# Performance work log

Measured on AMD Instinct MI355X. Metric: run time of the kernel, lower is better.

The kernel has to match this reference:

```python
import jax, jax.numpy as jnp
import numpy as np
import math

NUM_LEVEL = 16
LEVEL_DIM = 2
BASE_RES = 16
LOG2_T = 19
LEVEL_SCALE = 1.38191288
N_POINTS = 262144

_PRIMES = np.array([1, 2654435761, 805459861], dtype=np.uint32)  # tiny-cuda-nn hash primes
_CORNERS = np.array([[(c >> d) & 1 for d in range(3)] for c in range(8)], dtype=np.uint32)  # [8,3]


def _grid_meta():
    # mirrors GridEncoder.get_grid_info: per-level table offsets (aligned to 8)
    max_len = 2 ** LOG2_T
    offs = []
    off = 0
    for i in range(NUM_LEVEL):
        res = int(np.ceil(BASE_RES * LEVEL_SCALE ** i))
        p = min(max_len, res ** 3)
        p = int(np.ceil(p / 8) * 8)
        offs.append(off)
        off += p
    offs.append(off)
    return offs


def setup_inputs() -> dict:
    key = jax.random.key(0)
    k1, k2 = jax.random.split(key)
    offs = _grid_meta()
    # raw coords in [-1, 1); forward maps (x+1)/2 -> [0, 1)
    input_means = jax.random.uniform(k1, (N_POINTS, 3), dtype=jnp.float32) * 2.0 - 1.0
    # embeddings.data.uniform_(-0.01, 0.01)
    embeddings = jax.random.uniform(k2, (offs[-1], LEVEL_DIM), dtype=jnp.float32) * 0.02 - 0.01
    return {"input_means": input_means, "embeddings": embeddings}


def _encode(input_means, embeddings):
    x = (input_means + 1.0) / 2.0  # [N,3] in [0,1]
    offs = _grid_meta()
    lg_scale = math.log2(LEVEL_SCALE)
    corners = jnp.asarray(_CORNERS)  # [8,3]
    primes = jnp.asarray(_PRIMES)    # [3]
    outs = []
    for l in range(NUM_LEVEL):
        hsize = offs[l + 1] - offs[l]                    # table rows this level
        scale = 2.0 ** (l * lg_scale) * BASE_RES - 1.0   # align_corners=True
        res = int(math.ceil(scale)) + 1                  # grid resolution
        table = embeddings[offs[l]:offs[l + 1]]          # [hsize, C]
        pos = x * scale                                  # align_corners -> no +0.5
        pg = jnp.floor(pos)
        frac = pos - pg                                  # [N,3]
        pgu = pg.astype(jnp.uint32)
        cpos = pgu[:, None, :] + corners[None]           # [N,8,3] corner coords
        if res ** 3 > hsize:
            # hashed level: xor of coord*prime (uint32 wraparound)
            h = cpos * primes
            idx = h[..., 0] ^ h[..., 1] ^ h[..., 2]
        else:
            # dense (tiled) level
            r = jnp.uint32(res)
            idx = cpos[..., 0] + cpos[..., 1] * r + cpos[..., 2] * r * r
        idx = (idx % jnp.uint32(hsize)).astype(jnp.int32)
        feats = table[idx]                               # [N,8,C] gather
        w = jnp.where(corners[None] == 1, frac[:, None, :], 1.0 - frac[:, None, :]).prod(-1)  # [N,8]
        outs.append(jnp.einsum('nk,nkc->nc', w, feats))  # trilinear interp
    # matches ot_encod.permute(1,0,2).reshape(N, L*C): level-major feature concat
    return jnp.concatenate(outs, axis=-1)                # [N, L*C]


def reference(input_means, embeddings):
    return _encode(input_means, embeddings)
```

## Files before the change

kernel.cpp:

```cpp
#include <hip/hip_runtime.h>
#include <cmath>

#define NPTS 262144
#define NLVL 16
#define NDENSE 5
#define NHASH 11
#define HASH_MASK 0x7FFFFu
#define P2 2654435761u
#define P3 805459861u

typedef float v2f __attribute__((ext_vector_type(2)));
typedef float v3f __attribute__((ext_vector_type(3)));
typedef float v4f __attribute__((ext_vector_type(4)));
typedef float v4f8 __attribute__((ext_vector_type(4), aligned(8)));

struct MetaD { float scale[NDENSE]; unsigned off[NDENSE]; unsigned res[NDENSE]; };
struct MetaH { float scale[NHASH]; unsigned off[NHASH]; };

struct Pt { float x, y, z; };
struct Prep { unsigned idx[8]; float fx, fy, fz; };

__device__ __forceinline__ Pt load_pt_nt(const float* __restrict__ means, int p) {
    const v3f m = __builtin_nontemporal_load((const v3f*)(means + 3 * p));
    Pt q;
    q.x = (m.x + 1.0f) * 0.5f;
    q.y = (m.y + 1.0f) * 0.5f;
    q.z = (m.z + 1.0f) * 0.5f;
    return q;
}

__device__ __forceinline__ Prep hprep(Pt q, float s, unsigned off) {
    const float px = q.x * s, py = q.y * s, pz = q.z * s;
    const float gx = floorf(px), gy = floorf(py), gz = floorf(pz);
    Prep d;
    d.fx = px - gx; d.fy = py - gy; d.fz = pz - gz;
    const unsigned ix = (unsigned)gx, iy = (unsigned)gy, iz = (unsigned)gz;
    const unsigned hy0 = iy * P2, hy1 = hy0 + P2;
    const unsigned hz0 = iz * P3, hz1 = hz0 + P3;
    const unsigned h0 = hy0 ^ hz0, h1 = hy1 ^ hz0, h2 = hy0 ^ hz1, h3 = hy1 ^ hz1;
    d.idx[0] = ((ix ^ h0) & HASH_MASK) + off; d.idx[1] = (((ix + 1u) ^ h0) & HASH_MASK) + off;
    d.idx[2] = ((ix ^ h1) & HASH_MASK) + off; d.idx[3] = (((ix + 1u) ^ h1) & HASH_MASK) + off;
    d.idx[4] = ((ix ^ h2) & HASH_MASK) + off; d.idx[5] = (((ix + 1u) ^ h2) & HASH_MASK) + off;
    d.idx[6] = ((ix ^ h3) & HASH_MASK) + off; d.idx[7] = (((ix + 1u) ^ h3) & HASH_MASK) + off;
    return d;
}

__device__ __forceinline__ v2f trilerp(const v2f* f, float fx, float fy, float fz) {
    const float wx0 = 1.0f - fx, wy0 = 1.0f - fy, wz0 = 1.0f - fz;
    const float w00 = wz0 * wy0, w01 = wz0 * fy, w10 = fz * wy0, w11 = fz * fy;
    return w00 * (wx0 * f[0] + fx * f[1]) + w01 * (wx0 * f[2] + fx * f[3])
         + w10 * (wx0 * f[4] + fx * f[5]) + w11 * (wx0 * f[6] + fx * f[7]);
}

__global__ __launch_bounds__(256) void enc_hash(
    const float* __restrict__ means, const float* __restrict__ emb,
    v2f* __restrict__ dst, int lvl_major, MetaH meta)
{
    const unsigned b = blockIdx.x;
    const unsigned xcd = b & 7u, slot = b >> 3;
    unsigned il, chunk;
    if (slot < 512u) { il = xcd; chunk = slot; }
    else {
        const unsigned g = xcd * 192u + (slot - 512u);
        il = 8u + (g >> 9);
        chunk = g & 511u;
    }
    const float s = meta.scale[il];
    const unsigned off = meta.off[il];
    const unsigned lvl = il + NDENSE;
    const int p0 = (int)(chunk * 512u + threadIdx.x);
    const v2f* __restrict__ emb2 = (const v2f*)emb;

    const Prep A = hprep(load_pt_nt(means, p0), s, off);
    v2f fa[8];
#pragma unroll
    for (int k = 0; k < 8; ++k) fa[k] = emb2[A.idx[k]];
    const Prep B = hprep(load_pt_nt(means, p0 + 256), s, off);
    v2f fb[8];
#pragma unroll
    for (int k = 0; k < 8; ++k) fb[k] = emb2[B.idx[k]];

    const v2f ra = trilerp(fa, A.fx, A.fy, A.fz);
    const size_t diA = lvl_major ? ((size_t)lvl * NPTS + p0) : ((size_t)p0 * NLVL + lvl);
    dst[diA] = ra;
    const v2f rb = trilerp(fb, B.fx, B.fy, B.fz);
    const size_t diB = lvl_major ? ((size_t)lvl * NPTS + (p0 + 256)) : ((size_t)(p0 + 256) * NLVL + lvl);
    dst[diB] = rb;
}

__global__ __launch_bounds__(256) void finalize(
    const float* __restrict__ means, const float* __restrict__ emb,
    const v2f* __restrict__ ws, float* __restrict__ out, MetaD meta)
{
    const int p = blockIdx.x * 256 + threadIdx.x;

    v2f h[NHASH];
#pragma unroll
    for (int l = 0; l < NHASH; ++l)
        h[l] = ws[(size_t)(NDENSE + l) * NPTS + p];

    const Pt q = load_pt_nt(means, p);

    v4f o[8];
    v2f* o2 = (v2f*)o;
#pragma unroll
    for (int l = 0; l < NDENSE; ++l) {
        const float s = meta.scale[l];
        const unsigned off = meta.off[l];
        const unsigned r = meta.res[l];
        const float px = q.x * s, py = q.y * s, pz = q.z * s;
        const float gx = floorf(px), gy = floorf(py), gz = floorf(pz);
        const float fx = px - gx, fy = py - gy, fz = pz - gz;
        const unsigned dy = r, dz = r * r;
        const unsigned base = (unsigned)gx + (unsigned)gy * dy + (unsigned)gz * dz + off;

        v4f8 F[4];
        F[0] = *(const v4f8*)(emb + 2u * base);
        F[1] = *(const v4f8*)(emb + 2u * (base + dy));
        F[2] = *(const v4f8*)(emb + 2u * (base + dz));
        F[3] = *(const v4f8*)(emb + 2u * (base + dz + dy));

        const float wx0 = 1.0f - fx, wy0 = 1.0f - fy, wz0 = 1.0f - fz;
        const float wc[4] = {wz0 * wy0, wz0 * fy, fz * wy0, fz * fy};
        v2f acc = {0.0f, 0.0f};
#pragma unroll
        for (int c = 0; c < 4; ++c)
            acc += wc[c] * (wx0 * (v2f){F[c].x, F[c].y} + fx * (v2f){F[c].z, F[c].w});
        o2[l] = acc;
    }
#pragma unroll
    for (int l = 0; l < NHASH; ++l)
        o2[NDENSE + l] = h[l];

    v4f* out4 = (v4f*)(out + (size_t)p * (2 * NLVL));
#pragma unroll
    for (int k = 0; k < 8; ++k)
        __builtin_nontemporal_store(o[k], &out4[k]);
}

__global__ __launch_bounds__(256) void enc_dense(
    const float* __restrict__ means, const float* __restrict__ emb,
    v2f* __restrict__ dst, int lvl_major, MetaD meta)
{
    const int p = blockIdx.x * 256 + threadIdx.x;
    const int l = blockIdx.y;

    const Pt q = load_pt_nt(means, p);
    const float s = meta.scale[l];
    const unsigned off = meta.off[l];
    const unsigned r = meta.res[l];

    const float px = q.x * s, py = q.y * s, pz = q.z * s;
    const float gx = floorf(px), gy = floorf(py), gz = floorf(pz);
    const float fx = px - gx, fy = py - gy, fz = pz - gz;
    const unsigned dy = r, dz = r * r;
    const unsigned base = (unsigned)gx + (unsigned)gy * dy + (unsigned)gz * dz + off;

    v4f8 F[4];
    F[0] = *(const v4f8*)(emb + 2u * base);
    F[1] = *(const v4f8*)(emb + 2u * (base + dy));
    F[2] = *(const v4f8*)(emb + 2u * (base + dz));
    F[3] = *(const v4f8*)(emb + 2u * (base + dz + dy));

    const float wx0 = 1.0f - fx, wy0 = 1.0f - fy, wz0 = 1.0f - fz;
    const float wc[4] = {wz0 * wy0, wz0 * fy, fz * wy0, fz * fy};
    v2f acc = {0.0f, 0.0f};
#pragma unroll
    for (int c = 0; c < 4; ++c)
        acc += wc[c] * (wx0 * (v2f){F[c].x, F[c].y} + fx * (v2f){F[c].z, F[c].w});

    const size_t di = lvl_major ? ((size_t)l * NPTS + p) : ((size_t)p * NLVL + l);
    dst[di] = acc;
}

extern "C" void kernel_launch(void* const* d_in, const int* in_sizes, int n_in,
                              void* d_out, int out_size, void* d_ws, size_t ws_size,
                              hipStream_t stream)
{
    const float* means = (const float*)d_in[0];
    const float* emb   = (const float*)d_in[1];
    float* out         = (float*)d_out;

    MetaD md;
    MetaH mh;
    const double lg = log2(1.38191288);
    unsigned off = 0;
    for (int l = 0; l < NLVL; ++l) {
        const double scale_d = pow(2.0, (double)l * lg) * 16.0 - 1.0;
        const unsigned res_enc = (unsigned)ceil(scale_d) + 1u;

        const double gres_d = ceil(16.0 * pow(1.38191288, (double)l));
        unsigned long long r3 = (unsigned long long)gres_d;
        r3 = r3 * r3 * r3;
        unsigned long long pl = r3 < (1ull << 19) ? r3 : (1ull << 19);
        pl = (pl + 7ull) / 8ull * 8ull;

        if (l < NDENSE) {
            md.scale[l] = (float)scale_d;
            md.off[l]   = off;
            md.res[l]   = res_enc;
        } else {
            mh.scale[l - NDENSE] = (float)scale_d;
            mh.off[l - NDENSE]   = off;
        }
        off += (unsigned)pl;
    }

    const size_t ws_needed = (size_t)NLVL * NPTS * sizeof(float) * 2;
    const bool use_ws = ws_size >= ws_needed;

    if (use_ws) {
        v2f* wsp = (v2f*)d_ws;
        enc_hash<<<dim3(8 * 704, 1, 1), 256, 0, stream>>>(means, emb, wsp, 1, mh);
        finalize<<<NPTS / 256, 256, 0, stream>>>(means, emb, (const v2f*)wsp, out, md);
    } else {
        v2f* dst = (v2f*)out;
        enc_dense<<<dim3(NPTS / 256, NDENSE, 1), 256, 0, stream>>>(means, emb, dst, 0, md);
        enc_hash <<<dim3(8 * 704, 1, 1),          256, 0, stream>>>(means, emb, dst, 0, mh);
    }
}
```

Before: 210.0 us.

## Stage first two dense level tables in LDS for finalize kernel

The finalize kernel now copies the embedding rows of dense levels 0 and 1 (about 127 KB) into shared memory per 1024-thread block, then reads their corner features from LDS instead of global memory. The point coordinate loads also drop the nontemporal hint and use a 4-byte-aligned vector type. The aim is to cut global/L2 gather traffic for the small dense levels. In exchange, each of the 256 blocks must first copy the whole table, and the large LDS footprint allows only one block per CU, which limits occupancy and latency hiding.

```diff
diff --git a/kernel.cpp b/kernel.cpp
--- a/kernel.cpp
+++ b/kernel.cpp
@@ -9,8 +9,11 @@
 #define P2 2654435761u
 #define P3 805459861u
 
+#define DENSE01_F4 8132
+#define DENSE01_BYTES 130112
+
 typedef float v2f __attribute__((ext_vector_type(2)));
-typedef float v3f __attribute__((ext_vector_type(3)));
+typedef float v3f __attribute__((ext_vector_type(3), aligned(4)));
 typedef float v4f __attribute__((ext_vector_type(4)));
 typedef float v4f8 __attribute__((ext_vector_type(4), aligned(8)));
 
@@ -20,8 +23,8 @@
 struct Pt { float x, y, z; };
 struct Prep { unsigned idx[8]; float fx, fy, fz; };
 
-__device__ __forceinline__ Pt load_pt_nt(const float* __restrict__ means, int p) {
-    const v3f m = __builtin_nontemporal_load((const v3f*)(means + 3 * p));
+__device__ __forceinline__ Pt load_pt(const float* __restrict__ means, int p) {
+    const v3f m = *(const v3f*)(means + 3 * p);
     Pt q;
     q.x = (m.x + 1.0f) * 0.5f;
     q.y = (m.y + 1.0f) * 0.5f;
@@ -71,11 +74,11 @@
     const int p0 = (int)(chunk * 512u + threadIdx.x);
     const v2f* __restrict__ emb2 = (const v2f*)emb;
 
-    const Prep A = hprep(load_pt_nt(means, p0), s, off);
+    const Prep A = hprep(load_pt(means, p0), s, off);
     v2f fa[8];
 #pragma unroll
     for (int k = 0; k < 8; ++k) fa[k] = emb2[A.idx[k]];
-    const Prep B = hprep(load_pt_nt(means, p0 + 256), s, off);
+    const Prep B = hprep(load_pt(means, p0 + 256), s, off);
     v2f fb[8];
 #pragma unroll
     for (int k = 0; k < 8; ++k) fb[k] = emb2[B.idx[k]];
@@ -88,46 +91,69 @@
     dst[diB] = rb;
 }
 
-__global__ __launch_bounds__(256) void finalize(
-    const float* __restrict__ means, const float* __restrict__ emb,
-    const v2f* __restrict__ ws, float* __restrict__ out, MetaD meta)
-{
-    const int p = blockIdx.x * 256 + threadIdx.x;
-
-    v2f h[NHASH];
-#pragma unroll
-    for (int l = 0; l < NHASH; ++l)
-        h[l] = ws[(size_t)(NDENSE + l) * NPTS + p];
-
-    const Pt q = load_pt_nt(means, p);
-
-    v4f o[8];
-    v2f* o2 = (v2f*)o;
-#pragma unroll
-    for (int l = 0; l < NDENSE; ++l) {
-        const float s = meta.scale[l];
-        const unsigned off = meta.off[l];
-        const unsigned r = meta.res[l];
-        const float px = q.x * s, py = q.y * s, pz = q.z * s;
-        const float gx = floorf(px), gy = floorf(py), gz = floorf(pz);
-        const float fx = px - gx, fy = py - gy, fz = pz - gz;
-        const unsigned dy = r, dz = r * r;
-        const unsigned base = (unsigned)gx + (unsigned)gy * dy + (unsigned)gz * dz + off;
-
+__device__ __forceinline__ v2f dense_level(
+    const Pt& q, const float* __restrict__ emb, const v2f* __restrict__ lds2,
+    bool use_lds, float s, unsigned r, unsigned off)
+{
+    const float px = q.x * s, py = q.y * s, pz = q.z * s;
+    const float gx = floorf(px), gy = floorf(py), gz = floorf(pz);
+    const float fx = px - gx, fy = py - gy, fz = pz - gz;
+    const unsigned dy = r, dz = r * r;
+    const unsigned base = (unsigned)gx + (unsigned)gy * dy + (unsigned)gz * dz + off;
+
+    const float wx0 = 1.0f - fx, wy0 = 1.0f - fy, wz0 = 1.0f - fz;
+    const float wc[4] = {wz0 * wy0, wz0 * fy, fz * wy0, fz * fy};
+    v2f acc = {0.0f, 0.0f};
+    if (use_lds) {
+        const unsigned bi[4] = {base, base + dy, base + dz, base + dz + dy};
+#pragma unroll
+        for (int c = 0; c < 4; ++c)
+            acc += wc[c] * (wx0 * lds2[bi[c]] + fx * lds2[bi[c] + 1]);
+    } else {
         v4f8 F[4];
         F[0] = *(const v4f8*)(emb + 2u * base);
         F[1] = *(const v4f8*)(emb + 2u * (base + dy));
         F[2] = *(const v4f8*)(emb + 2u * (base + dz));
         F[3] = *(const v4f8*)(emb + 2u * (base + dz + dy));
-
-        const float wx0 = 1.0f - fx, wy0 = 1.0f - fy, wz0 = 1.0f - fz;
-        const float wc[4] = {wz0 * wy0, wz0 * fy, fz * wy0, fz * fy};
-        v2f acc = {0.0f, 0.0f};
 #pragma unroll
         for (int c = 0; c < 4; ++c)
             acc += wc[c] * (wx0 * (v2f){F[c].x, F[c].y} + fx * (v2f){F[c].z, F[c].w});
-        o2[l] = acc;
-    }
+    }
+    return acc;
+}
+
+__global__ __launch_bounds__(1024) void finalize_lds(
+    const float* __restrict__ means, const float* __restrict__ emb,
+    const v2f* __restrict__ ws, float* __restrict__ out, MetaD meta)
+{
+    extern __shared__ float lds[];
+    const int t = threadIdx.x;
+    {
+        const v4f* __restrict__ src4 = (const v4f*)emb;
+        v4f* dst4 = (v4f*)lds;
+#pragma unroll
+        for (int k = 0; k < 8; ++k) {
+            const int i = t + (k << 10);
+            if (i < DENSE01_F4) dst4[i] = src4[i];
+        }
+    }
+    __syncthreads();
+    const v2f* __restrict__ lds2 = (const v2f*)lds;
+
+    const int p = blockIdx.x * 1024 + t;
+
+    v2f h[NHASH];
+#pragma unroll
+    for (int l = 0; l < NHASH; ++l)
+        h[l] = ws[(size_t)(NDENSE + l) * NPTS + p];
+
+    const Pt q = load_pt(means, p);
+
+    v4f o[8];
+    v2f* o2 = (v2f*)o;
+#pragma unroll
+    for (int l = 0; l < NDENSE; ++l)
+        o2[l] = dense_level(q, emb, lds2, l < 2, meta.scale[l], meta.res[l], meta.off[l]);
 #pragma unroll
     for (int l = 0; l < NHASH; ++l)
         o2[NDENSE + l] = h[l];
@@ -138,39 +164,44 @@
         __builtin_nontemporal_store(o[k], &out4[k]);
 }
 
+__global__ __launch_bounds__(256) void finalize_g(
+    const float* __restrict__ means, const float* __restrict__ emb,
+    const v2f* __restrict__ ws, float* __restrict__ out, MetaD meta)
+{
+    const int p = blockIdx.x * 256 + threadIdx.x;
+
+    v2f h[NHASH];
+#pragma unroll
+    for (int l = 0; l < NHASH; ++l)
+        h[l] = ws[(size_t)(NDENSE + l) * NPTS + p];
+
+    const Pt q = load_pt(means, p);
+
+    v4f o[8];
+    v2f* o2 = (v2f*)o;
+#pragma unroll
+    for (int l = 0; l < NDENSE; ++l)
+        o2[l] = dense_level(q, emb, nullptr, false, meta.scale[l], meta.res[l], meta.off[l]);
+#pragma unroll
+    for (int l = 0; l < NHASH; ++l)
+        o2[NDENSE + l] = h[l];
+
+    v4f* out4 = (v4f*)(out + (size_t)p * (2 * NLVL));
+#pragma unroll
+    for (int k = 0; k < 8; ++k)
+        __builtin_nontemporal_store(o[k], &out4[k]);
+}
+
 __global__ __launch_bounds__(256) void enc_dense(
     const float* __restrict__ means, const float* __restrict__ emb,
     v2f* __restrict__ dst, int lvl_major, MetaD meta)
 {
     const int p = blockIdx.x * 256 + threadIdx.x;
     const int l = blockIdx.y;
-
-    const Pt q = load_pt_nt(means, p);
-    const float s = meta.scale[l];
-    const unsigned off = meta.off[l];
-    const unsigned r = meta.res[l];
-
-    const float px = q.x * s, py = q.y * s, pz = q.z * s;
-    const float gx = floorf(px), gy = floorf(py), gz = floorf(pz);
-    const float fx = px - gx, fy = py - gy, fz = pz - gz;
-    const unsigned dy = r, dz = r * r;
-    const unsigned base = (unsigned)gx + (unsigned)gy * dy + (unsigned)gz * dz + off;
-
-    v4f8 F[4];
-    F[0] = *(const v4f8*)(emb + 2u * base);
-    F[1] = *(const v4f8*)(emb + 2u * (base + dy));
-    F[2] = *(const v4f8*)(emb + 2u * (base + dz));
-    F[3] = *(const v4f8*)(emb + 2u * (base + dz + dy));
-
-    const float wx0 = 1.0f - fx, wy0 = 1.0f - fy, wz0 = 1.0f - fz;
-    const float wc[4] = {wz0 * wy0, wz0 * fy, fz * wy0, fz * fy};
-    v2f acc = {0.0f, 0.0f};
-#pragma unroll
-    for (int c = 0; c < 4; ++c)
-        acc += wc[c] * (wx0 * (v2f){F[c].x, F[c].y} + fx * (v2f){F[c].z, F[c].w});
-
+    const Pt q = load_pt(means, p);
+    const v2f res = dense_level(q, emb, nullptr, false, meta.scale[l], meta.res[l], meta.off[l]);
     const size_t di = lvl_major ? ((size_t)l * NPTS + p) : ((size_t)p * NLVL + l);
-    dst[di] = acc;
+    dst[di] = res;
 }
 
 extern "C" void kernel_launch(void* const* d_in, const int* in_sizes, int n_in,
@@ -206,13 +237,23 @@
         off += (unsigned)pl;
     }
 
+    static int lds_ok = -1;
+    if (lds_ok < 0) {
+        lds_ok = (hipFuncSetAttribute((const void*)finalize_lds,
+                                      hipFuncAttributeMaxDynamicSharedMemorySize,
+                                      DENSE01_BYTES) == hipSuccess) ? 1 : 0;
+    }
+
     const size_t ws_needed = (size_t)NLVL * NPTS * sizeof(float) * 2;
     const bool use_ws = ws_size >= ws_needed;
 
     if (use_ws) {
         v2f* wsp = (v2f*)d_ws;
         enc_hash<<<dim3(8 * 704, 1, 1), 256, 0, stream>>>(means, emb, wsp, 1, mh);
-        finalize<<<NPTS / 256, 256, 0, stream>>>(means, emb, (const v2f*)wsp, out, md);
+        if (lds_ok)
+            finalize_lds<<<NPTS / 1024, 1024, DENSE01_BYTES, stream>>>(means, emb, (const v2f*)wsp, out, md);
+        else
+            finalize_g<<<NPTS / 256, 256, 0, stream>>>(means, emb, (const v2f*)wsp, out, md);
     } else {
         v2f* dst = (v2f*)out;
         enc_dense<<<dim3(NPTS / 256, NDENSE, 1), 256, 0, stream>>>(means, emb, dst, 0, md);
```

New measurement: 230.0 us. 1.1x slower.
